# Kernel optimization log

Hardware: AMD Instinct MI355X
Metric: run time of the kernel (lower is better)

The kernel has to match this reference:

```python
import jax, jax.numpy as jnp
from jax import lax
import numpy as np

B, H, W, C = 64, 64, 64, 8          # batch, grid, channel_n (C=8 is structurally required)
PC = 3 * C                           # perceive output channels = 24
FIRE_RATE = 0.5
ALPHA_THR = 0.1

def _conv(x, w, b, padding):
    y = lax.conv_general_dilated(x, w, (1, 1), padding,
                                 dimension_numbers=('NHWC', 'HWIO', 'NHWC'))
    return y + b

def _dwconv(x, k):
    # k: [kh, kw, Cin, mult] (TF depthwise layout) -> grouped conv rhs [kh, kw, 1, Cin*mult]
    kh, kw, cin, m = k.shape
    rhs = k.reshape(kh, kw, 1, cin * m)
    return lax.conv_general_dilated(x, rhs, (1, 1), 'SAME',
                                    dimension_numbers=('NHWC', 'HWIO', 'NHWC'),
                                    feature_group_count=cin)

def _maxpool3(a):
    return lax.reduce_window(a, -jnp.inf, lax.max, (1, 3, 3, 1), (1, 1, 1, 1), 'SAME')

def setup_inputs() -> dict:
    key = jax.random.key(0)
    ks = jax.random.split(key, 12)
    d_flat = H * W * PC                       # 98304
    d_att = 3 * 3 * 24 * 3                    # 648
    s = lambda *sh: 0.02
    return {
        'x': jax.random.normal(ks[0], (B, H, W, C), jnp.float32),
        'update_noise': jax.random.uniform(ks[1], (B, H, W, 1), jnp.float32),
        'W_att': jax.random.normal(ks[2], (d_flat, d_att), jnp.float32) * 0.002,
        'b_att': jax.random.normal(ks[3], (d_att,), jnp.float32) * 0.02,
        'W1': jax.random.normal(ks[4], (3, 3, 3 * PC, 48), jnp.float32) * 0.05,
        'b1': jax.random.normal(ks[5], (48,), jnp.float32) * 0.02,
        'Wt': jax.random.normal(ks[6], (3, 3, 48, 48), jnp.float32) * 0.05,
        'bt': jax.random.normal(ks[7], (48,), jnp.float32) * 0.02,
        'W2': jax.random.normal(ks[8], (1, 1, 48, 128), jnp.float32) * 0.05,
        'b2': jax.random.normal(ks[9], (128,), jnp.float32) * 0.02,
        'W3': jax.random.normal(ks[10], (1, 1, 128, C), jnp.float32) * 0.05,
        'b3': jax.random.normal(ks[11], (C,), jnp.float32) * 0.02,
    }

def reference(x, update_noise, W_att, b_att, W1, b1, Wt, bt, W2, b2, W3, b3):
    # --- fixed perceive stencil (angle = 0) ---
    ident = np.outer(np.float32([0, 1, 0]), np.float32([0, 1, 0]))
    dxk = np.outer(np.float32([1, 0, 1]), np.float32([1, 0, 1])) / 8.0
    dyk = dxk.T
    k = jnp.stack([jnp.asarray(ident), jnp.asarray(dxk), jnp.asarray(dyk)], -1)  # [3,3,3]
    k = jnp.tile(k[:, :, None, :], (1, 1, C, 1))                                 # [3,3,C,3]

    pre_life = _maxpool3(x[:, :, :, 3:4]) > ALPHA_THR

    y = _dwconv(x, k)                                     # [B,H,W,24]
    # global attention: flatten -> dense -> reshape, take sample 0's kernel
    y_sum = (y.reshape(y.shape[0], -1) @ W_att + b_att).reshape(-1, 3, 3, 24, 3)[0]
    y = _dwconv(y, y_sum)                                 # [B,H,W,72]
    y = y * lax.rsqrt(jnp.maximum(jnp.sum(y * y), 1e-12))  # global l2_normalize

    # dmodel: conv3 VALID -> convT3 VALID -> 1x1 relu -> 1x1
    h = _conv(y, W1, b1, 'VALID')                         # [B,62,62,48]
    h = lax.conv_transpose(h, Wt, (1, 1), 'VALID',
                           dimension_numbers=('NHWC', 'HWIO', 'NHWC')) + bt  # [B,64,64,48]
    h = jax.nn.relu(_conv(h, W2, b2, 'SAME'))             # [B,64,64,128]
    dx_out = _conv(h, W3, b3, 'SAME')                     # [B,64,64,C], step_size = 1.0

    update_mask = (update_noise <= FIRE_RATE).astype(x.dtype)
    x2 = x + dx_out * update_mask

    post_life = _maxpool3(x2[:, :, :, 3:4]) > ALPHA_THR
    life = jnp.logical_and(pre_life, post_life).astype(x.dtype)
    return x2 * life
```

## Files before the change

### kernel.cpp

```cpp
#include <hip/hip_runtime.h>

#define NB 64
#define HW 4096

typedef __attribute__((ext_vector_type(8))) short short8;
typedef __attribute__((ext_vector_type(4))) float f32x4;

__device__ __forceinline__ unsigned short bf16_rn(float v) {
  unsigned int u = __float_as_uint(v);
  return (unsigned short)((u + 0x7fffu + ((u >> 16) & 1u)) >> 16);
}

__global__ __launch_bounds__(256) void k_perceive(
    const float* __restrict__ x, float* __restrict__ y_chw,
    float* __restrict__ y0_hwc, float* __restrict__ prelife,
    float* __restrict__ att_zero, const float* __restrict__ W2,
    float* __restrict__ W2T) {
  int t = threadIdx.x;
  if (blockIdx.x == 1024) {
    for (int i = t; i < 6144; i += 256) {
      int o = i / 48;
      int c = i - o * 48;
      W2T[i] = W2[c * 128 + o];
    }
    return;
  }
  if (blockIdx.x == 0) {
    for (int i = t; i < 649; i += 256) att_zero[i] = 0.f;
  }
  int pix = blockIdx.x * 256 + t;
  int b = pix >> 12;
  int hw = pix & 4095;
  int h = hw >> 6, w = hw & 63;
  const float* xp = x + (size_t)pix * 8;
  bool hm = h > 0, hp = h < 63, wm = w > 0, wp = w < 63;

  float mx = -1e30f;
  #pragma unroll
  for (int di = -1; di <= 1; ++di) {
    if ((unsigned)(h + di) > 63u) continue;
    #pragma unroll
    for (int dj = -1; dj <= 1; ++dj) {
      if ((unsigned)(w + dj) > 63u) continue;
      mx = fmaxf(mx, xp[(di * 64 + dj) * 8 + 3]);
    }
  }
  prelife[pix] = (mx > 0.1f) ? 1.f : 0.f;

  float* yb = y_chw + (size_t)b * 16 * HW + hw;
  bool b0 = (b == 0);
  #pragma unroll
  for (int c = 0; c < 8; ++c) {
    float ctr = xp[c];
    float a00 = (hm && wm) ? xp[(-65) * 8 + c] : 0.f;
    float a02 = (hm && wp) ? xp[(-63) * 8 + c] : 0.f;
    float a20 = (hp && wm) ? xp[(63) * 8 + c] : 0.f;
    float a22 = (hp && wp) ? xp[(65) * 8 + c] : 0.f;
    float d = (a00 + a02 + a20 + a22) * 0.125f;
    yb[(size_t)(c * 2 + 0) * HW] = ctr;
    yb[(size_t)(c * 2 + 1) * HW] = d;
    if (b0) {
      float* y0p = y0_hwc + hw * 24 + c * 3;
      y0p[0] = ctr; y0p[1] = d; y0p[2] = d;
    }
  }
}

__global__ __launch_bounds__(256) void k_att(
    const float* __restrict__ y0, const float* __restrict__ Watt,
    float* __restrict__ att_acc) {
  int t = threadIdx.x;
  int r0 = blockIdx.x * 64;
  float a0 = 0.f, a1 = 0.f, a2 = 0.f;
  float b0 = 0.f, b1 = 0.f, b2 = 0.f;
  for (int r = 0; r < 64; r += 2) {
    float yv0 = y0[r0 + r];
    float yv1 = y0[r0 + r + 1];
    const float* w0 = Watt + (size_t)(r0 + r) * 648;
    const float* w1 = w0 + 648;
    a0 = fmaf(yv0, w0[t], a0);
    b0 = fmaf(yv1, w1[t], b0);
    a1 = fmaf(yv0, w0[t + 256], a1);
    b1 = fmaf(yv1, w1[t + 256], b1);
    if (t < 136) {
      a2 = fmaf(yv0, w0[t + 512], a2);
      b2 = fmaf(yv1, w1[t + 512], b2);
    }
  }
  atomicAdd(att_acc + t, a0 + b0);
  atomicAdd(att_acc + t + 256, a1 + b1);
  if (t < 136) atomicAdd(att_acc + t + 512, a2 + b2);
}

__global__ __launch_bounds__(256) void k_ssqfold(
    const float* __restrict__ y_chw, const float* __restrict__ att_acc,
    const float* __restrict__ b_att, float* __restrict__ ssq,
    const float* __restrict__ W1, unsigned short* __restrict__ K16H,
    unsigned short* __restrict__ K16L) {
  __shared__ float ys[648];
  __shared__ float s[16 * 324];
  int t = threadIdx.x;

  if (blockIdx.x >= 1024) {
    for (int i = t; i < 648; i += 256) ys[i] = att_acc[i] + b_att[i];
    __syncthreads();
    int r = blockIdx.x - 1024;
    int ri = r / 5, rj = r - ri * 5;
    #pragma unroll
    for (int k = 0; k < 3; ++k) {
      int idx = t + 256 * k;
      int p = idx / 48;
      int o = idx - p * 48;
      int c = p >> 1, tt = p & 1;
      float acc = 0.f;
      for (int ki = 0; ki < 3; ++ki) {
        int qi = ri - ki;
        if ((unsigned)qi > 2u) continue;
        for (int kj = 0; kj < 3; ++kj) {
          int qj = rj - kj;
          if ((unsigned)qj > 2u) continue;
          int k9 = ki * 3 + kj, q9 = qi * 3 + qj;
          const float* wb = W1 + (size_t)(k9 * 72 + 9 * c) * 48 + o;
          const float* yb = ys + q9 * 72 + 9 * c;
          if (tt == 0) {
            #pragma unroll
            for (int m = 0; m < 3; ++m) acc = fmaf(wb[(size_t)m * 48], yb[m], acc);
          } else {
            #pragma unroll
            for (int m = 0; m < 3; ++m) {
              acc = fmaf(wb[(size_t)(3 + m) * 48], yb[3 + m], acc);
              acc = fmaf(wb[(size_t)(6 + m) * 48], yb[6 + m], acc);
            }
          }
        }
      }
      unsigned short hb_ = bf16_rn(acc);
      float fhi = __uint_as_float(((unsigned int)hb_) << 16);
      unsigned short lb_ = bf16_rn(acc - fhi);
      K16H[o * 416 + r * 16 + p] = hb_;
      K16L[o * 416 + r * 16 + p] = lb_;
      if (r == 24) {
        K16H[o * 416 + 400 + p] = 0;
        K16L[o * 416 + 400 + p] = 0;
      }
    }
    return;
  }

  for (int i = t; i < 648; i += 256) ys[i] = att_acc[i] + b_att[i];

  int blk = blockIdx.x;
  int b = blk >> 4;
  int tile = blk & 15;
  int i0 = (tile >> 2) * 16;
  int j0 = (tile & 3) * 16;
  const float* yb = y_chw + (size_t)b * 16 * HW;

  for (int idx = t; idx < 16 * 324; idx += 256) {
    int c = idx / 324;
    int pos = idx - c * 324;
    int r = pos / 18, col = pos - r * 18;
    int gr = i0 - 1 + r, gc = j0 - 1 + col;
    bool v = ((unsigned)gr < 64u) && ((unsigned)gc < 64u);
    s[idx] = v ? yb[(size_t)c * HW + gr * 64 + gc] : 0.f;
  }
  __syncthreads();

  int ty = t >> 4, tx = t & 15;
  float local = 0.f;
  for (int c = 0; c < 8; ++c) {
    float tapA[9], tapB[9];
    const float* sa = s + (size_t)(2 * c) * 324 + ty * 18 + tx;
    const float* sb = s + (size_t)(2 * c + 1) * 324 + ty * 18 + tx;
    #pragma unroll
    for (int di = 0; di < 3; ++di)
      #pragma unroll
      for (int dj = 0; dj < 3; ++dj) {
        tapA[di * 3 + dj] = sa[di * 18 + dj];
        tapB[di * 3 + dj] = sb[di * 18 + dj];
      }
    #pragma unroll
    for (int m = 0; m < 3; ++m) {
      float z0 = 0.f, z1 = 0.f, z2 = 0.f;
      #pragma unroll
      for (int k9 = 0; k9 < 9; ++k9) {
        z0 = fmaf(tapA[k9], ys[k9 * 72 + 9 * c + m], z0);
        z1 = fmaf(tapB[k9], ys[k9 * 72 + 9 * c + 3 + m], z1);
        z2 = fmaf(tapB[k9], ys[k9 * 72 + 9 * c + 6 + m], z2);
      }
      local += z0 * z0 + z1 * z1 + z2 * z2;
    }
  }
  #pragma unroll
  for (int off = 32; off; off >>= 1) local += __shfl_down(local, off, 64);
  if ((t & 63) == 0) atomicAdd(ssq, local);
}

__global__ __launch_bounds__(256, 4) void k_conv1f(
    const float* __restrict__ y_chw, const unsigned short* __restrict__ K16H,
    const unsigned short* __restrict__ K16L, const float* __restrict__ b1,
    const float* __restrict__ ssqp, float* __restrict__ h1) {
  __shared__ short sh[2 * 6656];
  int t = threadIdx.x;
  int w = t >> 6, lane = t & 63;
  int blk = blockIdx.x;
  int b = blk >> 4;
  int tile = blk & 15;
  int i0 = (tile >> 2) * 16; if (i0 > 46) i0 = 46;
  int j0 = (tile & 3) * 16;  if (j0 > 46) j0 = 46;

  const float* yb = y_chw + (size_t)b * 16 * HW;
  for (int idx = t; idx < 16 * 400; idx += 256) {
    int c = idx / 400;
    int pos = idx - c * 400;
    int r = pos / 20, col = pos - r * 20;
    int gr = i0 - 1 + r, gc = j0 - 1 + col;
    bool v = ((unsigned)gr < 64u) && ((unsigned)gc < 64u);
    float val = v ? yb[(size_t)c * HW + gr * 64 + gc] : 0.f;
    unsigned short hb_ = bf16_rn(val);
    float fhi = __uint_as_float(((unsigned int)hb_) << 16);
    unsigned short lb_ = bf16_rn(val - fhi);
    sh[pos * 16 + c] = (short)hb_;
    sh[6656 + pos * 16 + c] = (short)lb_;
  }
  if (t < 256) {
    sh[6400 + t] = 0;
    sh[6656 + 6400 + t] = 0;
  }
  __syncthreads();

  f32x4 acc[4][3];
  #pragma unroll
  for (int m = 0; m < 4; ++m)
    #pragma unroll
    for (int n = 0; n < 3; ++n) acc[m][n] = (f32x4){0.f, 0.f, 0.f, 0.f};

  int lanecol = lane & 15;
  int half = (lane >> 4) >> 1;
  int c0 = ((lane >> 4) & 1) * 8;

  for (int ks = 0; ks < 13; ++ks) {
    short8 bh[3], bl[3];
    #pragma unroll
    for (int n = 0; n < 3; ++n) {
      int o = n * 16 + lanecol;
      size_t boff = (size_t)o * 416 + ks * 32 + (lane >> 4) * 8;
      bh[n] = *(const short8*)(K16H + boff);
      bl[n] = *(const short8*)(K16L + boff);
    }
    int tap = 2 * ks + half;
    int ri = tap / 5, rj = tap - ri * 5;
    int aoff = (ri * 20 + rj + lanecol) * 16 + c0;
    #pragma unroll
    for (int m = 0; m < 4; ++m) {
      int mt = (w << 2) + m;
      int ao = aoff + mt * 320;
      short8 ah = *(const short8*)(sh + ao);
      short8 al = *(const short8*)(sh + 6656 + ao);
      #pragma unroll
      for (int n = 0; n < 3; ++n) {
        acc[m][n] = __builtin_amdgcn_mfma_f32_16x16x32_bf16(ah, bh[n], acc[m][n], 0, 0, 0);
        acc[m][n] = __builtin_amdgcn_mfma_f32_16x16x32_bf16(ah, bl[n], acc[m][n], 0, 0, 0);
        acc[m][n] = __builtin_amdgcn_mfma_f32_16x16x32_bf16(al, bh[n], acc[m][n], 0, 0, 0);
      }
    }
  }

  float inv = rsqrtf(fmaxf(ssqp[0], 1e-12f));
  int rg = lane >> 4;
  #pragma unroll
  for (int n = 0; n < 3; ++n) {
    int o = n * 16 + lanecol;
    float bo = b1[o];
    #pragma unroll
    for (int m = 0; m < 4; ++m) {
      int mt = (w << 2) + m;
      float* hp = h1 + ((size_t)b * 48 + o) * 3844 + (i0 + mt) * 62 + j0 + rg * 4;
      #pragma unroll
      for (int r = 0; r < 4; ++r) hp[r] = fmaf(acc[m][n][r], inv, bo);
    }
  }
}

__global__ __launch_bounds__(256, 4) void k_convTh(
    const float* __restrict__ h1, const float* __restrict__ Wt,
    const float* __restrict__ bt, const float* __restrict__ W2T,
    const float* __restrict__ b2, const float* __restrict__ W3,
    const float* __restrict__ b3, const float* __restrict__ x,
    const float* __restrict__ noise, float* __restrict__ x2,
    float* __restrict__ alpha2) {
  __shared__ float s[24 * 324];
  int t = threadIdx.x;
  int og = __builtin_amdgcn_readfirstlane(t >> 7);
  int sub = t & 127;
  int ty = sub >> 4, tx = sub & 15;
  int blk = blockIdx.x;
  int b = blk >> 4;
  int tile = blk & 15;
  int i0 = (tile >> 2) * 16;
  int j0 = (tile & 3) * 16;

  float acc0[24], acc1[24];
  #pragma unroll
  for (int o = 0; o < 24; ++o) { acc0[o] = 0.f; acc1[o] = 0.f; }
  const float* hb = h1 + (size_t)b * 48 * 3844;

  for (int c0 = 0; c0 < 48; c0 += 24) {
    __syncthreads();
    for (int idx = t; idx < 24 * 324; idx += 256) {
      int c = idx / 324;
      int pos = idx - c * 324;
      int r = pos / 18, col = pos - r * 18;
      int gr = i0 - 2 + r, gc = j0 - 2 + col;
      bool v = ((unsigned)gr < 62u) && ((unsigned)gc < 62u);
      s[idx] = v ? hb[(size_t)(c0 + c) * 3844 + gr * 62 + gc] : 0.f;
    }
    __syncthreads();
    for (int c = 0; c < 24; ++c) {
      const float* sc = s + c * 324 + ty * 18 + tx;
      float tap0[9], tap1[9];
      #pragma unroll
      for (int di = 0; di < 3; ++di)
        #pragma unroll
        for (int dj = 0; dj < 3; ++dj) {
          tap0[di * 3 + dj] = sc[di * 18 + dj];
          tap1[di * 3 + dj] = sc[(di + 8) * 18 + dj];
        }
      #pragma unroll
      for (int k9 = 0; k9 < 9; ++k9) {
        const float* w = Wt + (size_t)(k9 * 48 + c0 + c) * 48 + og * 24;
        float tv0 = tap0[k9], tv1 = tap1[k9];
        #pragma unroll
        for (int o = 0; o < 24; ++o) {
          acc0[o] = fmaf(tv0, w[o], acc0[o]);
          acc1[o] = fmaf(tv1, w[o], acc1[o]);
        }
      }
    }
  }

  float hr[48];
  #pragma unroll
  for (int ph = 0; ph < 2; ++ph) {
    __syncthreads();
    if (og == ph) {
      #pragma unroll
      for (int o = 0; o < 24; ++o) {
        float bo = bt[ph * 24 + o];
        s[o * 256 + ty * 16 + tx] = acc0[o] + bo;
        s[o * 256 + (ty + 8) * 16 + tx] = acc1[o] + bo;
      }
    }
    __syncthreads();
    #pragma unroll
    for (int c = 0; c < 24; ++c) hr[ph * 24 + c] = s[c * 256 + t];
  }

  int pty = t >> 4, ptx = t & 15;
  int pix = b * 4096 + (i0 + pty) * 64 + (j0 + ptx);
  float dx[8];
  #pragma unroll
  for (int k = 0; k < 8; ++k) dx[k] = b3[k];
  #pragma unroll 4
  for (int o = 0; o < 128; ++o) {
    float v = b2[o];
    const float* w2 = W2T + o * 48;
    #pragma unroll
    for (int c = 0; c < 48; ++c) v = fmaf(hr[c], w2[c], v);
    v = fmaxf(v, 0.f);
    const float* w3 = W3 + o * 8;
    #pragma unroll
    for (int k = 0; k < 8; ++k) dx[k] = fmaf(v, w3[k], dx[k]);
  }
  float m = (noise[pix] <= 0.5f) ? 1.f : 0.f;
  const float* xp = x + (size_t)pix * 8;
  float* xo = x2 + (size_t)pix * 8;
  float a3 = 0.f;
  #pragma unroll
  for (int k = 0; k < 8; ++k) {
    float v = fmaf(dx[k], m, xp[k]);
    xo[k] = v;
    if (k == 3) a3 = v;
  }
  alpha2[pix] = a3;
}

__global__ __launch_bounds__(256) void k_life(
    const float* __restrict__ x2, const float* __restrict__ alpha2,
    const float* __restrict__ prelife, float* __restrict__ out) {
  int pix = blockIdx.x * 256 + threadIdx.x;
  int hw = pix & 4095;
  int h = hw >> 6, w = hw & 63;
  const float* ab = alpha2 + (size_t)(pix - hw);
  float mx = -1e30f;
  #pragma unroll
  for (int di = -1; di <= 1; ++di) {
    if ((unsigned)(h + di) > 63u) continue;
    #pragma unroll
    for (int dj = -1; dj <= 1; ++dj) {
      if ((unsigned)(w + dj) > 63u) continue;
      mx = fmaxf(mx, ab[(h + di) * 64 + (w + dj)]);
    }
  }
  float life = (mx > 0.1f && prelife[pix] > 0.5f) ? 1.f : 0.f;
  const float* xp = x2 + (size_t)pix * 8;
  float* op = out + (size_t)pix * 8;
  #pragma unroll
  for (int k = 0; k < 8; ++k) op[k] = xp[k] * life;
}

extern "C" void kernel_launch(void* const* d_in, const int* in_sizes, int n_in,
                              void* d_out, int out_size, void* d_ws, size_t ws_size,
                              hipStream_t stream) {
  const float* x     = (const float*)d_in[0];
  const float* noise = (const float*)d_in[1];
  const float* Watt  = (const float*)d_in[2];
  const float* b_att = (const float*)d_in[3];
  const float* W1    = (const float*)d_in[4];
  const float* b1    = (const float*)d_in[5];
  const float* Wt    = (const float*)d_in[6];
  const float* bt    = (const float*)d_in[7];
  const float* W2    = (const float*)d_in[8];
  const float* b2    = (const float*)d_in[9];
  const float* W3    = (const float*)d_in[10];
  const float* b3    = (const float*)d_in[11];
  float* out = (float*)d_out;

  float* ws = (float*)d_ws;
  size_t o_y   = 0;
  size_t o_h1  = o_y + 4194304;
  size_t o_y0  = o_h1 + 11808768;
  size_t o_pre = o_y0 + 98304;
  size_t o_att = o_pre + 262144;
  size_t o_w2t = o_att + 652;
  size_t o_kh  = o_w2t + 6144;
  size_t o_kl  = o_kh + 9984;
  float* y_chw   = ws + o_y;
  float* h1_chw  = ws + o_h1;
  float* y0_hwc  = ws + o_y0;
  float* prelife = ws + o_pre;
  float* att_acc = ws + o_att;
  float* ssq     = ws + o_att + 648;
  float* W2T     = ws + o_w2t;
  unsigned short* K16H = (unsigned short*)(ws + o_kh);
  unsigned short* K16L = (unsigned short*)(ws + o_kl);
  float* x2      = ws + o_y;
  float* alpha2  = ws + o_y + 2097152;

  k_perceive<<<1025, 256, 0, stream>>>(x, y_chw, y0_hwc, prelife, att_acc, W2, W2T);
  k_att<<<1536, 256, 0, stream>>>(y0_hwc, Watt, att_acc);
  k_ssqfold<<<1049, 256, 0, stream>>>(y_chw, att_acc, b_att, ssq, W1, K16H, K16L);
  k_conv1f<<<1024, 256, 0, stream>>>(y_chw, K16H, K16L, b1, ssq, h1_chw);
  k_convTh<<<1024, 256, 0, stream>>>(h1_chw, Wt, bt, W2T, b2, W3, b3, x, noise, x2, alpha2);
  k_life<<<1024, 256, 0, stream>>>(x2, alpha2, prelife, out);
}
```

Baseline: 753.2 us.

## Compute transposed conv in k_convTh with split-bf16 MFMA instead of scalar FMA

The 3x3 transposed convolution in k_convTh is rewritten as an implicit GEMM on bf16 MFMA 16x16x32 instructions, replacing the scalar FP32 FMA loops. Each FP32 value is split into high and low bf16 parts and three products are accumulated to keep near-FP32 accuracy. The weights are pre-split and reordered once in the setup block of k_perceive. The input tile is stored in shared memory in channel-last layout so the A fragments can be loaded as vectors. This trades extra conversion work and three MFMAs per product for a large cut in scalar FMA count.

Measured after the change: 801.4 us. 1.06x slower.

```diff
diff --git a/kernel.cpp b/kernel.cpp
--- a/kernel.cpp
+++ b/kernel.cpp
@@ -15,13 +15,27 @@
     const float* __restrict__ x, float* __restrict__ y_chw,
     float* __restrict__ y0_hwc, float* __restrict__ prelife,
     float* __restrict__ att_zero, const float* __restrict__ W2,
-    float* __restrict__ W2T) {
+    float* __restrict__ W2T, const float* __restrict__ Wt,
+    unsigned short* __restrict__ WtH, unsigned short* __restrict__ WtL) {
   int t = threadIdx.x;
   if (blockIdx.x == 1024) {
     for (int i = t; i < 6144; i += 256) {
       int o = i / 48;
       int c = i - o * 48;
       W2T[i] = W2[c * 128 + o];
+    }
+    for (int i = t; i < 48 * 448; i += 256) {
+      int o = i / 448;
+      int kk = i - o * 448;
+      int phase = kk / 224;
+      int k2 = kk - phase * 224;
+      int tap = k2 / 24;
+      int cc = k2 - tap * 24;
+      float val = (tap < 9) ? Wt[(size_t)(tap * 48 + phase * 24 + cc) * 48 + o] : 0.f;
+      unsigned short hb_ = bf16_rn(val);
+      float fhi = __uint_as_float(((unsigned int)hb_) << 16);
+      WtH[i] = hb_;
+      WtL[i] = bf16_rn(val - fhi);
     }
     return;
   }
@@ -283,77 +297,92 @@
 }
 
 __global__ __launch_bounds__(256, 4) void k_convTh(
-    const float* __restrict__ h1, const float* __restrict__ Wt,
-    const float* __restrict__ bt, const float* __restrict__ W2T,
-    const float* __restrict__ b2, const float* __restrict__ W3,
-    const float* __restrict__ b3, const float* __restrict__ x,
-    const float* __restrict__ noise, float* __restrict__ x2,
-    float* __restrict__ alpha2) {
-  __shared__ float s[24 * 324];
+    const float* __restrict__ h1, const unsigned short* __restrict__ WtH,
+    const unsigned short* __restrict__ WtL, const float* __restrict__ bt,
+    const float* __restrict__ W2T, const float* __restrict__ b2,
+    const float* __restrict__ W3, const float* __restrict__ b3,
+    const float* __restrict__ x, const float* __restrict__ noise,
+    float* __restrict__ x2, float* __restrict__ alpha2) {
+  __shared__ float sf[7776];
+  short* shH = (short*)sf;
+  short* shL = ((short*)sf) + 7776;
   int t = threadIdx.x;
-  int og = __builtin_amdgcn_readfirstlane(t >> 7);
-  int sub = t & 127;
-  int ty = sub >> 4, tx = sub & 15;
+  int w = t >> 6, lane = t & 63;
+  int lanecol = lane & 15, f = lane >> 4;
   int blk = blockIdx.x;
   int b = blk >> 4;
   int tile = blk & 15;
   int i0 = (tile >> 2) * 16;
   int j0 = (tile & 3) * 16;
 
-  float acc0[24], acc1[24];
-  #pragma unroll
-  for (int o = 0; o < 24; ++o) { acc0[o] = 0.f; acc1[o] = 0.f; }
+  f32x4 acc[4][3];
+  #pragma unroll
+  for (int m = 0; m < 4; ++m)
+    #pragma unroll
+    for (int n = 0; n < 3; ++n) acc[m][n] = (f32x4){0.f, 0.f, 0.f, 0.f};
   const float* hb = h1 + (size_t)b * 48 * 3844;
 
-  for (int c0 = 0; c0 < 48; c0 += 24) {
+  for (int phase = 0; phase < 2; ++phase) {
     __syncthreads();
-    for (int idx = t; idx < 24 * 324; idx += 256) {
+    for (int idx = t; idx < 7776; idx += 256) {
       int c = idx / 324;
       int pos = idx - c * 324;
       int r = pos / 18, col = pos - r * 18;
       int gr = i0 - 2 + r, gc = j0 - 2 + col;
       bool v = ((unsigned)gr < 62u) && ((unsigned)gc < 62u);
-      s[idx] = v ? hb[(size_t)(c0 + c) * 3844 + gr * 62 + gc] : 0.f;
+      float val = v ? hb[(size_t)(phase * 24 + c) * 3844 + gr * 62 + gc] : 0.f;
+      unsigned short hbb = bf16_rn(val);
+      float fhi = __uint_as_float(((unsigned int)hbb) << 16);
+      unsigned short lbb = bf16_rn(val - fhi);
+      shH[pos * 24 + c] = (short)hbb;
+      shL[pos * 24 + c] = (short)lbb;
     }
     __syncthreads();
-    for (int c = 0; c < 24; ++c) {
-      const float* sc = s + c * 324 + ty * 18 + tx;
-      float tap0[9], tap1[9];
-      #pragma unroll
-      for (int di = 0; di < 3; ++di)
+    #pragma unroll
+    for (int ks = 0; ks < 7; ++ks) {
+      short8 bh[3], bl[3];
+      #pragma unroll
+      for (int n = 0; n < 3; ++n) {
+        int o = n * 16 + lanecol;
+        size_t boff = (size_t)o * 448 + phase * 224 + ks * 32 + f * 8;
+        bh[n] = *(const short8*)(WtH + boff);
+        bl[n] = *(const short8*)(WtL + boff);
+      }
+      int u = ks * 4 + f;
+      int tap = u / 3;
+      int cc0 = (u - 3 * tap) * 8;
+      int tc = tap < 9 ? tap : 8;
+      int di = tc / 3, dj = tc - di * 3;
+      #pragma unroll
+      for (int m = 0; m < 4; ++m) {
+        int mt = (w << 2) + m;
+        int ao = ((mt + di) * 18 + lanecol + dj) * 24 + cc0;
+        short8 ah = *(const short8*)(shH + ao);
+        short8 al = *(const short8*)(shL + ao);
         #pragma unroll
-        for (int dj = 0; dj < 3; ++dj) {
-          tap0[di * 3 + dj] = sc[di * 18 + dj];
-          tap1[di * 3 + dj] = sc[(di + 8) * 18 + dj];
+        for (int n = 0; n < 3; ++n) {
+          acc[m][n] = __builtin_amdgcn_mfma_f32_16x16x32_bf16(ah, bh[n], acc[m][n], 0, 0, 0);
+          acc[m][n] = __builtin_amdgcn_mfma_f32_16x16x32_bf16(ah, bl[n], acc[m][n], 0, 0, 0);
+          acc[m][n] = __builtin_amdgcn_mfma_f32_16x16x32_bf16(al, bh[n], acc[m][n], 0, 0, 0);
         }
-      #pragma unroll
-      for (int k9 = 0; k9 < 9; ++k9) {
-        const float* w = Wt + (size_t)(k9 * 48 + c0 + c) * 48 + og * 24;
-        float tv0 = tap0[k9], tv1 = tap1[k9];
-        #pragma unroll
-        for (int o = 0; o < 24; ++o) {
-          acc0[o] = fmaf(tv0, w[o], acc0[o]);
-          acc1[o] = fmaf(tv1, w[o], acc1[o]);
-        }
       }
     }
   }
 
   float hr[48];
   #pragma unroll
-  for (int ph = 0; ph < 2; ++ph) {
+  for (int n = 0; n < 3; ++n) {
     __syncthreads();
-    if (og == ph) {
-      #pragma unroll
-      for (int o = 0; o < 24; ++o) {
-        float bo = bt[ph * 24 + o];
-        s[o * 256 + ty * 16 + tx] = acc0[o] + bo;
-        s[o * 256 + (ty + 8) * 16 + tx] = acc1[o] + bo;
-      }
+    #pragma unroll
+    for (int m = 0; m < 4; ++m) {
+      int mt = (w << 2) + m;
+      #pragma unroll
+      for (int r = 0; r < 4; ++r)
+        sf[lanecol * 257 + mt * 16 + f * 4 + r] = acc[m][n][r] + bt[n * 16 + lanecol];
     }
     __syncthreads();
     #pragma unroll
-    for (int c = 0; c < 24; ++c) hr[ph * 24 + c] = s[c * 256 + t];
+    for (int c = 0; c < 16; ++c) hr[n * 16 + c] = sf[c * 257 + t];
   }
 
   int pty = t >> 4, ptx = t & 15;
@@ -435,6 +464,8 @@
   size_t o_w2t = o_att + 652;
   size_t o_kh  = o_w2t + 6144;
   size_t o_kl  = o_kh + 9984;
+  size_t o_wth = o_kl + 9984;
+  size_t o_wtl = o_wth + 10752;
   float* y_chw   = ws + o_y;
   float* h1_chw  = ws + o_h1;
   float* y0_hwc  = ws + o_y0;
@@ -444,13 +475,15 @@
   float* W2T     = ws + o_w2t;
   unsigned short* K16H = (unsigned short*)(ws + o_kh);
   unsigned short* K16L = (unsigned short*)(ws + o_kl);
+  unsigned short* WtH  = (unsigned short*)(ws + o_wth);
+  unsigned short* WtL  = (unsigned short*)(ws + o_wtl);
   float* x2      = ws + o_y;
   float* alpha2  = ws + o_y + 2097152;
 
-  k_perceive<<<1025, 256, 0, stream>>>(x, y_chw, y0_hwc, prelife, att_acc, W2, W2T);
+  k_perceive<<<1025, 256, 0, stream>>>(x, y_chw, y0_hwc, prelife, att_acc, W2, W2T, Wt, WtH, WtL);
   k_att<<<1536, 256, 0, stream>>>(y0_hwc, Watt, att_acc);
   k_ssqfold<<<1049, 256, 0, stream>>>(y_chw, att_acc, b_att, ssq, W1, K16H, K16L);
   k_conv1f<<<1024, 256, 0, stream>>>(y_chw, K16H, K16L, b1, ssq, h1_chw);
-  k_convTh<<<1024, 256, 0, stream>>>(h1_chw, Wt, bt, W2T, b2, W3, b3, x, noise, x2, alpha2);
+  k_convTh<<<1024, 256, 0, stream>>>(h1_chw, WtH, WtL, bt, W2T, b2, W3, b3, x, noise, x2, alpha2);
   k_life<<<1024, 256, 0, stream>>>(x2, alpha2, prelife, out);
 }
```
